# Optimization experiments

Measured on AMD Instinct MI355X. Metric: run time of the kernel, lower is better.

## Reference

```python
import jax, jax.numpy as jnp
import numpy as np

NH = 16  # attention heads
TOPK = 50

def _rms(x, w):
    return x * jax.lax.rsqrt(jnp.mean(x * x, axis=-1, keepdims=True) + 1e-6) * w

def _rope(x, pos):
    # x: [1, T, NH, HD], pos: [T]
    half = x.shape[-1] // 2
    inv = 1.0 / (10000.0 ** (jnp.arange(half, dtype=jnp.float32) / half))
    ang = pos.astype(jnp.float32)[:, None] * inv[None, :]          # [T, half]
    cos = jnp.cos(ang)[None, :, None, :]
    sin = jnp.sin(ang)[None, :, None, :]
    x1, x2 = x[..., :half], x[..., half:]
    return jnp.concatenate([x1 * cos - x2 * sin, x2 * cos + x1 * sin], axis=-1)


def setup_inputs() -> dict:
    key = jax.random.key(0)
    ks = jax.random.split(key, 12)
    G, V, D, NL, FF = 15, 2048, 1024, 2, 4096
    s = 0.02
    return {
        'talker_hidden': jax.random.normal(ks[0], (1, 1, D), jnp.float32),
        'code_0_embed': jax.random.normal(ks[1], (1, 1, D), jnp.float32),
        'temperature': jnp.ones((1,), jnp.float32),
        'sample_uniforms': jax.random.uniform(ks[2], (G,), jnp.float32),
        'stacked_heads': jax.random.normal(ks[3], (G, V, D), jnp.float32) * s,
        'stacked_embeds': jax.random.normal(ks[4], (G, V, D), jnp.float32) * s,
        'ln1': jnp.ones((NL, D), jnp.float32),
        'ln2': jnp.ones((NL, D), jnp.float32),
        'ln_f': jnp.ones((D,), jnp.float32),
        'wq': jax.random.normal(ks[5], (NL, D, D), jnp.float32) * s,
        'wk': jax.random.normal(ks[6], (NL, D, D), jnp.float32) * s,
        'wv': jax.random.normal(ks[7], (NL, D, D), jnp.float32) * s,
        'wo': jax.random.normal(ks[8], (NL, D, D), jnp.float32) * s,
        'w1': jax.random.normal(ks[9], (NL, D, FF), jnp.float32) * s,
        'w2': jax.random.normal(ks[10], (NL, FF, D), jnp.float32) * s,
    }


def reference(talker_hidden, code_0_embed, temperature, sample_uniforms,
              stacked_heads, stacked_embeds, ln1, ln2, ln_f,
              wq, wk, wv, wo, w1, w2):
    NL = wq.shape[0]
    D = wq.shape[1]
    HD = D // NH
    G = stacked_heads.shape[0]

    def transformer_step(h, qpos, caches):
        # h: [1, T, D]; qpos: [T] absolute positions; caches: list of (k,v) or None
        new_caches = []
        for l in range(NL):
            T = h.shape[1]
            x = _rms(h, ln1[l])
            q = (x @ wq[l]).reshape(1, T, NH, HD)
            k = (x @ wk[l]).reshape(1, T, NH, HD)
            v = (x @ wv[l]).reshape(1, T, NH, HD)
            q = _rope(q, qpos)
            k = _rope(k, qpos)
            if caches is None:
                k_all, v_all = k, v
            else:
                k_all = jnp.concatenate([caches[l][0], k], axis=1)
                v_all = jnp.concatenate([caches[l][1], v], axis=1)
            new_caches.append((k_all, v_all))
            S = k_all.shape[1]
            scores = jnp.einsum('bthd,bshd->bhts', q, k_all) / jnp.sqrt(jnp.float32(HD))
            mask = jnp.arange(S)[None, :] <= qpos[:, None]      # [T, S] causal
            scores = jnp.where(mask[None, None], scores, jnp.float32(-1e30))
            attn = jax.nn.softmax(scores, axis=-1)
            out = jnp.einsum('bhts,bshd->bthd', attn, v_all).reshape(1, T, D)
            h = h + out @ wo[l]
            h = h + jax.nn.gelu((_rms(h, ln2[l])) @ w1[l]) @ w2[l]
        return _rms(h, ln_f), new_caches

    cp_input = jnp.concatenate([talker_hidden, code_0_embed], axis=1)  # [1, 2, D]
    h_seq, caches = transformer_step(cp_input, jnp.arange(2), None)
    hidden = h_seq[:, -1:, :]                                           # [1, 1, D]

    safe_temp = jnp.maximum(temperature.reshape(()), 1e-5)
    embed_sum = code_0_embed.reshape(-1)
    codes = []
    for g in range(G):
        logits = stacked_heads[g] @ hidden.reshape(-1)                  # [V]
        topv, topi = jax.lax.top_k(logits, TOPK)
        probs = jax.nn.softmax(topv / safe_temp)
        cdf = jnp.cumsum(probs)
        u = jnp.clip(sample_uniforms[g], 1e-6, 1.0 - 1e-6)
        choice = jnp.argmax((cdf >= u).astype(jnp.int32))
        code = topi[choice]
        codes.append(code.astype(jnp.int64))
        emb = stacked_embeds[g][code]                                   # [D]
        embed_sum = embed_sum + emb
        if g + 1 < G:
            h_seq, caches = transformer_step(emb[None, None, :],
                                             jnp.array([g + 2]), caches)
            hidden = h_seq[:, -1:, :]
    return jnp.stack(codes), embed_sum
```

## Files before the change

### kernel.cpp

```cpp
#include <hip/hip_runtime.h>
#include <math.h>

#define D      1024
#define NHEADS 16
#define HDIM   64
#define NL     2
#define FF     4096
#define NGRP   15
#define VOC    2048
#define TOPK   50
#define MAXS   16

__device__ __forceinline__ float wave_reduce_sum(float v) {
#pragma unroll
    for (int m = 32; m >= 1; m >>= 1) v += __shfl_xor(v, m, 64);
    return v;
}

__device__ __forceinline__ float geluf(float y) {
    return 0.5f * y * (1.f + tanhf(0.7978845608028654f * (y + 0.044715f * y * y * y)));
}

__device__ __forceinline__ void load_rms(const float* __restrict__ src,
                                         const float* __restrict__ w,
                                         float* xn, float* red) {
    int tid = threadIdx.x;
    float ss = 0.f;
    for (int i = tid; i < D; i += 256) { float v = src[i]; xn[i] = v; ss += v * v; }
    red[tid] = ss;
    __syncthreads();
    for (int s = 128; s > 0; s >>= 1) {
        if (tid < s) red[tid] += red[tid + s];
        __syncthreads();
    }
    float inv = rsqrtf(red[0] / (float)D + 1e-6f);
    for (int i = tid; i < D; i += 256) xn[i] = xn[i] * inv * w[i];
    __syncthreads();
}

__global__ void k_init(const float* __restrict__ th, const float* __restrict__ c0,
                       float* __restrict__ h, float* __restrict__ out,
                       float* __restrict__ qkv) {
    int i = blockIdx.x * 256 + threadIdx.x;
    h[i] = th[i];
    h[D + i] = c0[i];
    out[NGRP + i] = c0[i];
#pragma unroll
    for (int j = 0; j < 6; ++j) qkv[j * 1024 + i] = 0.f;
}

__global__ void k_qkv(const float* __restrict__ h, const float* __restrict__ ln,
                      const float* __restrict__ Wq, const float* __restrict__ Wk,
                      const float* __restrict__ Wv, float* __restrict__ qkv) {
    __shared__ float xn[D];
    __shared__ float red[256];
    __shared__ float4 part[4][64];
    int t = blockIdx.z;
    int m = blockIdx.x >> 2, ob = blockIdx.x & 3;
    load_rms(h + t * D, ln, xn, red);
    const float* W = (m == 0) ? Wq : (m == 1) ? Wk : Wv;
    int tid = threadIdx.x, w = tid >> 6, lane = tid & 63;
    int obase = ob * 256;
    int kbase = (blockIdx.y * 4 + w) * 32;
    const float* Wp = W + (long)kbase * D + obase + lane * 4;
    float4 acc = {0.f, 0.f, 0.f, 0.f};
#pragma unroll 4
    for (int i = 0; i < 32; ++i) {
        float xv = xn[kbase + i];
        float4 wv = *(const float4*)(Wp + (long)i * D);
        acc.x += xv * wv.x; acc.y += xv * wv.y; acc.z += xv * wv.z; acc.w += xv * wv.w;
    }
    part[w][lane] = acc;
    __syncthreads();
    const float* p = (const float*)part;
    float s = p[tid] + p[256 + tid] + p[512 + tid] + p[768 + tid];
    atomicAdd(&qkv[t * 3 * D + m * D + obase + tid], s);
}

__global__ void k_attn(const float* __restrict__ qkv, float* __restrict__ kc,
                       float* __restrict__ vc, float* __restrict__ ao,
                       float* __restrict__ ub, int basePos) {
    int t = blockIdx.x, hd = blockIdx.y, d = threadIdx.x;
    {
        int fb = blockIdx.x * NHEADS + blockIdx.y;
#pragma unroll
        for (int j = 0; j < 4; ++j) ub[fb * 256 + j * 64 + d] = 0.f;
    }
    int pos = basePos + t;
    int i = d & 31;
    float inv = __expf(-(float)i * (9.210340371976184f / 32.0f));
    float ang = (float)pos * inv;
    float cs = cosf(ang), sn = sinf(ang);

    float q = qkv[t * 3 * D + hd * HDIM + d];
    float qp = __shfl_xor(q, 32, 64);
    float qr = (d < 32) ? (q * cs - qp * sn) : (q * cs + qp * sn);

    float k0 = qkv[t * 3 * D + D + hd * HDIM + d];
    float kp = __shfl_xor(k0, 32, 64);
    float kr = (d < 32) ? (k0 * cs - kp * sn) : (k0 * cs + kp * sn);

    float v0 = qkv[t * 3 * D + 2 * D + hd * HDIM + d];
    kc[pos * D + hd * HDIM + d] = kr;
    vc[pos * D + hd * HDIM + d] = v0;

    float sc[MAXS];
#pragma unroll
    for (int s = 0; s < MAXS; ++s) {
        if (s > pos) break;
        float kv;
        if (s < basePos) {
            kv = kc[s * D + hd * HDIM + d];
        } else if (s == pos) {
            kv = kr;
        } else {
            float kk = qkv[(s - basePos) * 3 * D + D + hd * HDIM + d];
            float kkp = __shfl_xor(kk, 32, 64);
            float a2 = (float)s * inv;
            float c2 = cosf(a2), s2 = sinf(a2);
            kv = (d < 32) ? (kk * c2 - kkp * s2) : (kk * c2 + kkp * s2);
        }
        float dt = wave_reduce_sum(qr * kv);
        sc[s] = dt * 0.125f;
    }
    float mx = -1e30f;
#pragma unroll
    for (int s = 0; s < MAXS; ++s) { if (s > pos) break; mx = fmaxf(mx, sc[s]); }
    float l = 0.f;
#pragma unroll
    for (int s = 0; s < MAXS; ++s) { if (s > pos) break; sc[s] = expf(sc[s] - mx); l += sc[s]; }
    float o = 0.f;
#pragma unroll
    for (int s = 0; s < MAXS; ++s) {
        if (s > pos) break;
        float vv = (s < basePos) ? vc[s * D + hd * HDIM + d]
                                 : qkv[(s - basePos) * 3 * D + 2 * D + hd * HDIM + d];
        o += sc[s] * vv;
    }
    ao[t * D + hd * HDIM + d] = o / l;
}

__global__ void k_wo(const float* __restrict__ ain, const float* __restrict__ W,
                     float* __restrict__ h, float* __restrict__ qkv) {
    __shared__ float xn[D];
    __shared__ float4 part[4][64];
    int t = blockIdx.z, tid = threadIdx.x;
    if (blockIdx.x == 0 && tid < 192)
        qkv[t * 3 * D + blockIdx.y * 192 + tid] = 0.f;
    for (int i = tid; i < D; i += 256) xn[i] = ain[t * D + i];
    __syncthreads();
    int w = tid >> 6, lane = tid & 63;
    int obase = blockIdx.x * 256;
    int kbase = (blockIdx.y * 4 + w) * 16;
    const float* Wp = W + (long)kbase * D + obase + lane * 4;
    float4 acc = {0.f, 0.f, 0.f, 0.f};
#pragma unroll 4
    for (int i = 0; i < 16; ++i) {
        float xv = xn[kbase + i];
        float4 wv = *(const float4*)(Wp + (long)i * D);
        acc.x += xv * wv.x; acc.y += xv * wv.y; acc.z += xv * wv.z; acc.w += xv * wv.w;
    }
    part[w][lane] = acc;
    __syncthreads();
    const float* p = (const float*)part;
    float s = p[tid] + p[256 + tid] + p[512 + tid] + p[768 + tid];
    atomicAdd(&h[t * D + obase + tid], s);
}

__global__ void k_ffn1(const float* __restrict__ h, const float* __restrict__ ln,
                       const float* __restrict__ W, float* __restrict__ ub) {
    __shared__ float xn[D];
    __shared__ float red[256];
    __shared__ float4 part[4][64];
    int t = blockIdx.z, tid = threadIdx.x;
    load_rms(h + t * D, ln, xn, red);
    int w = tid >> 6, lane = tid & 63;
    int obase = blockIdx.x * 256;
    int kbase = (blockIdx.y * 4 + w) * 32;
    const float* Wp = W + (long)kbase * FF + obase + lane * 4;
    float4 acc = {0.f, 0.f, 0.f, 0.f};
#pragma unroll 4
    for (int i = 0; i < 32; ++i) {
        float xv = xn[kbase + i];
        float4 wv = *(const float4*)(Wp + (long)i * FF);
        acc.x += xv * wv.x; acc.y += xv * wv.y; acc.z += xv * wv.z; acc.w += xv * wv.w;
    }
    part[w][lane] = acc;
    __syncthreads();
    const float* p = (const float*)part;
    float s = p[tid] + p[256 + tid] + p[512 + tid] + p[768 + tid];
    atomicAdd(&ub[t * FF + obase + tid], s);
}

__global__ void k_ffn2(const float* __restrict__ ub, const float* __restrict__ W,
                       float* __restrict__ h) {
    __shared__ float xs[128];
    __shared__ float4 part[4][64];
    int t = blockIdx.z, tid = threadIdx.x;
    int kblk = blockIdx.y * 128;
    if (tid < 128) xs[tid] = geluf(ub[t * FF + kblk + tid]);
    __syncthreads();
    int w = tid >> 6, lane = tid & 63;
    int obase = blockIdx.x * 256;
    int kloc = w * 32;
    const float* Wp = W + (long)(kblk + kloc) * D + obase + lane * 4;
    float4 acc = {0.f, 0.f, 0.f, 0.f};
#pragma unroll 4
    for (int i = 0; i < 32; ++i) {
        float xv = xs[kloc + i];
        float4 wv = *(const float4*)(Wp + (long)i * D);
        acc.x += xv * wv.x; acc.y += xv * wv.y; acc.z += xv * wv.z; acc.w += xv * wv.w;
    }
    part[w][lane] = acc;
    __syncthreads();
    const float* p = (const float*)part;
    float s = p[tid] + p[256 + tid] + p[512 + tid] + p[768 + tid];
    atomicAdd(&h[t * D + obase + tid], s);
}

__global__ void k_head(const float* __restrict__ h, const float* __restrict__ lnf,
                       const float* __restrict__ Hd, float* __restrict__ logits) {
    __shared__ float xn[D];
    __shared__ float red[256];
    load_rms(h, lnf, xn, red);
    int tid = threadIdx.x, lane = tid & 63, w = tid >> 6;
    int rbase = blockIdx.x * 16 + w * 4;
#pragma unroll
    for (int r = 0; r < 4; ++r) {
        const float* row = Hd + (long)(rbase + r) * D;
        float acc = 0.f;
#pragma unroll
        for (int it = 0; it < 4; ++it) {
            int idx = it * 256 + lane * 4;
            float4 a = *(const float4*)(row + idx);
            acc += a.x * xn[idx] + a.y * xn[idx + 1] + a.z * xn[idx + 2] + a.w * xn[idx + 3];
        }
        acc = wave_reduce_sum(acc);
        if (lane == 0) logits[rbase + r] = acc;
    }
}

__global__ void k_sample(const float* __restrict__ logits, const float* __restrict__ temp,
                         const float* __restrict__ unis, const float* __restrict__ embeds,
                         int g, float* __restrict__ h, float* __restrict__ out) {
    __shared__ float topv[TOPK];
    __shared__ int topi[TOPK];
    __shared__ int s_code;
    int tid = threadIdx.x;
    if (tid < 64) {
        int lane = tid;
        float v[32];
#pragma unroll
        for (int j = 0; j < 32; ++j) v[j] = logits[j * 64 + lane];
        for (int r = 0; r < TOPK; ++r) {
            float bv = v[0];
            int bj = 0;
#pragma unroll
            for (int j = 1; j < 32; ++j)
                if (v[j] > bv) { bv = v[j]; bj = j; }
            int bidx = bj * 64 + lane;
#pragma unroll
            for (int m = 32; m >= 1; m >>= 1) {
                float ov = __shfl_xor(bv, m, 64);
                int oi = __shfl_xor(bidx, m, 64);
                if (ov > bv || (ov == bv && oi < bidx)) { bv = ov; bidx = oi; }
            }
            if (lane == 0) { topv[r] = bv; topi[r] = bidx; }
            if ((bidx & 63) == lane) v[bidx >> 6] = -3.0e38f;
        }
    }
    __syncthreads();
    if (tid == 0) {
        float t = fmaxf(temp[0], 1e-5f);
        float m = topv[0] / t;
        float p[TOPK];
        float l = 0.f;
        for (int j = 0; j < TOPK; ++j) { p[j] = expf(topv[j] / t - m); l += p[j]; }
        float u = unis[g];
        u = fminf(fmaxf(u, 1e-6f), 1.f - 1e-6f);
        float cdf = 0.f;
        int choice = 0;
        bool found = false;
        for (int j = 0; j < TOPK; ++j) {
            cdf += p[j] / l;
            if (!found && cdf >= u) { choice = j; found = true; }
        }
        s_code = topi[choice];
        out[g] = (float)s_code;
    }
    __syncthreads();
    int code = s_code;
    const float* e = embeds + ((long)g * VOC + code) * D;
    for (int i = tid; i < D; i += 256) {
        float ev = e[i];
        out[NGRP + i] += ev;
        h[i] = ev;
    }
}

extern "C" void kernel_launch(void* const* d_in, const int* in_sizes, int n_in,
                              void* d_out, int out_size, void* d_ws, size_t ws_size,
                              hipStream_t stream) {
    const float* talker = (const float*)d_in[0];
    const float* code0  = (const float*)d_in[1];
    const float* temp   = (const float*)d_in[2];
    const float* unis   = (const float*)d_in[3];
    const float* heads  = (const float*)d_in[4];
    const float* embeds = (const float*)d_in[5];
    const float* ln1    = (const float*)d_in[6];
    const float* ln2    = (const float*)d_in[7];
    const float* lnf    = (const float*)d_in[8];
    const float* wq     = (const float*)d_in[9];
    const float* wk     = (const float*)d_in[10];
    const float* wv     = (const float*)d_in[11];
    const float* wo     = (const float*)d_in[12];
    const float* w1     = (const float*)d_in[13];
    const float* w2     = (const float*)d_in[14];
    float* out = (float*)d_out;

    float* ws   = (float*)d_ws;
    float* h    = ws;
    float* qkvb = ws + 2048;
    float* ao   = ws + 8192;
    float* kc   = ws + 10240;
    float* vc   = ws + 43008;
    float* ub   = ws + 75776;
    float* lg   = ws + 83968;

    auto step = [&](int T, int basePos) {
        for (int l = 0; l < NL; ++l) {
            k_qkv<<<dim3(12, 8, T), 256, 0, stream>>>(h, ln1 + l * D,
                wq + (long)l * D * D, wk + (long)l * D * D, wv + (long)l * D * D, qkvb);
            k_attn<<<dim3(T, NHEADS), 64, 0, stream>>>(qkvb, kc + (long)l * MAXS * D,
                vc + (long)l * MAXS * D, ao, ub, basePos);
            k_wo<<<dim3(4, 16, T), 256, 0, stream>>>(ao, wo + (long)l * D * D, h, qkvb);
            k_ffn1<<<dim3(16, 8, T), 256, 0, stream>>>(h, ln2 + l * D, w1 + (long)l * D * FF, ub);
            k_ffn2<<<dim3(4, 32, T), 256, 0, stream>>>(ub, w2 + (long)l * FF * D, h);
        }
    };

    k_init<<<4, 256, 0, stream>>>(talker, code0, h, out, qkvb);
    step(2, 0);
    for (int g = 0; g < NGRP; ++g) {
        const float* hid = h + ((g == 0) ? 1 : 0) * D;
        k_head<<<128, 256, 0, stream>>>(hid, lnf, heads + (long)g * VOC * D, lg);
        k_sample<<<1, 256, 0, stream>>>(lg, temp, unis, embeds, g, h, out);
        if (g + 1 < NGRP) step(1, g + 2);
    }
}
```

Measured before the change: 2.392 ms.

## Fuse all decoder steps into one persistent kernel with grid barriers

Replaces roughly 190 small kernel launches (five per layer per step plus head and sample per group) with a single persistent 256-block kernel. Stages are separated by an atomic-counter grid barrier instead of kernel boundaries. The aim is to remove launch overhead and inter-kernel gaps in this latency-bound decode loop. The trade-offs are that 256 co-resident blocks are required for the spin barrier not to deadlock, each barrier costs global atomics and spinning, and the sampling stage leaves most blocks idle.

```diff
diff --git a/kernel.cpp b/kernel.cpp
--- a/kernel.cpp
+++ b/kernel.cpp
@@ -10,6 +10,16 @@
 #define VOC    2048
 #define TOPK   50
 #define MAXS   16
+#define NB     256
+
+struct Params {
+    const float* talker; const float* code0; const float* temp; const float* unis;
+    const float* heads;  const float* embeds;
+    const float* ln1; const float* ln2; const float* lnf;
+    const float* wq; const float* wk; const float* wv; const float* wo;
+    const float* w1; const float* w2;
+    float* out; float* ws;
+};
 
 __device__ __forceinline__ float wave_reduce_sum(float v) {
 #pragma unroll
@@ -19,6 +29,18 @@
 
 __device__ __forceinline__ float geluf(float y) {
     return 0.5f * y * (1.f + tanhf(0.7978845608028654f * (y + 0.044715f * y * y * y)));
+}
+
+__device__ __forceinline__ void gsync(unsigned* cnt, unsigned target) {
+    __syncthreads();
+    if (threadIdx.x == 0) {
+        __threadfence();
+        atomicAdd(cnt, 1u);
+        while (__hip_atomic_load(cnt, __ATOMIC_RELAXED, __HIP_MEMORY_SCOPE_AGENT) < target)
+            __builtin_amdgcn_s_sleep(1);
+        __threadfence();
+    }
+    __syncthreads();
 }
 
 __device__ __forceinline__ void load_rms(const float* __restrict__ src,
@@ -38,263 +60,296 @@
     __syncthreads();
 }
 
-__global__ void k_init(const float* __restrict__ th, const float* __restrict__ c0,
-                       float* __restrict__ h, float* __restrict__ out,
-                       float* __restrict__ qkv) {
+__global__ __launch_bounds__(256) void k_pre(const float* __restrict__ th,
+                                             const float* __restrict__ c0,
+                                             float* __restrict__ h,
+                                             float* __restrict__ out,
+                                             float* __restrict__ qkv,
+                                             unsigned* __restrict__ bar) {
     int i = blockIdx.x * 256 + threadIdx.x;
-    h[i] = th[i];
-    h[D + i] = c0[i];
-    out[NGRP + i] = c0[i];
-#pragma unroll
-    for (int j = 0; j < 6; ++j) qkv[j * 1024 + i] = 0.f;
-}
-
-__global__ void k_qkv(const float* __restrict__ h, const float* __restrict__ ln,
-                      const float* __restrict__ Wq, const float* __restrict__ Wk,
-                      const float* __restrict__ Wv, float* __restrict__ qkv) {
+    if (i == 0) *bar = 0u;
+    if (i < 1024) {
+        h[i] = th[i];
+        h[D + i] = c0[i];
+        out[NGRP + i] = c0[i];
+    }
+    for (int j = i; j < 2 * 3 * D; j += 2048) qkv[j] = 0.f;
+}
+
+__global__ __launch_bounds__(256) void k_all(Params p) {
     __shared__ float xn[D];
     __shared__ float red[256];
     __shared__ float4 part[4][64];
-    int t = blockIdx.z;
-    int m = blockIdx.x >> 2, ob = blockIdx.x & 3;
-    load_rms(h + t * D, ln, xn, red);
-    const float* W = (m == 0) ? Wq : (m == 1) ? Wk : Wv;
-    int tid = threadIdx.x, w = tid >> 6, lane = tid & 63;
-    int obase = ob * 256;
-    int kbase = (blockIdx.y * 4 + w) * 32;
-    const float* Wp = W + (long)kbase * D + obase + lane * 4;
-    float4 acc = {0.f, 0.f, 0.f, 0.f};
+    __shared__ float s_topv[TOPK];
+    __shared__ int   s_topi[TOPK];
+    __shared__ int   s_code;
+
+    float* ws   = p.ws;
+    float* h    = ws;
+    float* qkvb = ws + 2048;
+    float* ao   = ws + 8192;
+    float* kc   = ws + 10240;
+    float* vc   = ws + 43008;
+    float* ub   = ws + 75776;
+    float* lg   = ws + 83968;
+    unsigned* bar = (unsigned*)(ws + 86016);
+
+    const int bid = blockIdx.x;
+    const int tid = threadIdx.x;
+    unsigned bt = 0;
+
+    auto step = [&](int T, int basePos) {
+        for (int l = 0; l < NL; ++l) {
+            if (bid < 96 * T) {
+                int x = bid % 12, y = (bid / 12) % 8, t = bid / 96;
+                int m = x >> 2, ob = x & 3;
+                load_rms(h + t * D, p.ln1 + l * D, xn, red);
+                const float* W = ((m == 0) ? p.wq : (m == 1) ? p.wk : p.wv) + (long)l * D * D;
+                int w = tid >> 6, lane = tid & 63;
+                int obase = ob * 256;
+                int kbase = (y * 4 + w) * 32;
+                const float* Wp = W + (long)kbase * D + obase + lane * 4;
+                float4 acc = {0.f, 0.f, 0.f, 0.f};
 #pragma unroll 4
-    for (int i = 0; i < 32; ++i) {
-        float xv = xn[kbase + i];
-        float4 wv = *(const float4*)(Wp + (long)i * D);
-        acc.x += xv * wv.x; acc.y += xv * wv.y; acc.z += xv * wv.z; acc.w += xv * wv.w;
-    }
-    part[w][lane] = acc;
-    __syncthreads();
-    const float* p = (const float*)part;
-    float s = p[tid] + p[256 + tid] + p[512 + tid] + p[768 + tid];
-    atomicAdd(&qkv[t * 3 * D + m * D + obase + tid], s);
-}
-
-__global__ void k_attn(const float* __restrict__ qkv, float* __restrict__ kc,
-                       float* __restrict__ vc, float* __restrict__ ao,
-                       float* __restrict__ ub, int basePos) {
-    int t = blockIdx.x, hd = blockIdx.y, d = threadIdx.x;
-    {
-        int fb = blockIdx.x * NHEADS + blockIdx.y;
-#pragma unroll
-        for (int j = 0; j < 4; ++j) ub[fb * 256 + j * 64 + d] = 0.f;
-    }
-    int pos = basePos + t;
-    int i = d & 31;
-    float inv = __expf(-(float)i * (9.210340371976184f / 32.0f));
-    float ang = (float)pos * inv;
-    float cs = cosf(ang), sn = sinf(ang);
-
-    float q = qkv[t * 3 * D + hd * HDIM + d];
-    float qp = __shfl_xor(q, 32, 64);
-    float qr = (d < 32) ? (q * cs - qp * sn) : (q * cs + qp * sn);
-
-    float k0 = qkv[t * 3 * D + D + hd * HDIM + d];
-    float kp = __shfl_xor(k0, 32, 64);
-    float kr = (d < 32) ? (k0 * cs - kp * sn) : (k0 * cs + kp * sn);
-
-    float v0 = qkv[t * 3 * D + 2 * D + hd * HDIM + d];
-    kc[pos * D + hd * HDIM + d] = kr;
-    vc[pos * D + hd * HDIM + d] = v0;
-
-    float sc[MAXS];
-#pragma unroll
-    for (int s = 0; s < MAXS; ++s) {
-        if (s > pos) break;
-        float kv;
-        if (s < basePos) {
-            kv = kc[s * D + hd * HDIM + d];
-        } else if (s == pos) {
-            kv = kr;
-        } else {
-            float kk = qkv[(s - basePos) * 3 * D + D + hd * HDIM + d];
-            float kkp = __shfl_xor(kk, 32, 64);
-            float a2 = (float)s * inv;
-            float c2 = cosf(a2), s2 = sinf(a2);
-            kv = (d < 32) ? (kk * c2 - kkp * s2) : (kk * c2 + kkp * s2);
+                for (int i = 0; i < 32; ++i) {
+                    float xv = xn[kbase + i];
+                    float4 wv4 = *(const float4*)(Wp + (long)i * D);
+                    acc.x += xv * wv4.x; acc.y += xv * wv4.y;
+                    acc.z += xv * wv4.z; acc.w += xv * wv4.w;
+                }
+                part[w][lane] = acc;
+                __syncthreads();
+                const float* pp = (const float*)part;
+                float s = pp[tid] + pp[256 + tid] + pp[512 + tid] + pp[768 + tid];
+                atomicAdd(&qkvb[t * 3 * D + m * D + obase + tid], s);
+            }
+            gsync(bar, bt += NB);
+
+            {
+                for (int i = bid * 256 + tid; i < T * FF; i += NB * 256) ub[i] = 0.f;
+                int wid = bid * 4 + (tid >> 6);
+                if (wid < T * NHEADS) {
+                    int t = wid / NHEADS, hd = wid % NHEADS, d = tid & 63;
+                    float* kcl = kc + (long)l * MAXS * D;
+                    float* vcl = vc + (long)l * MAXS * D;
+                    int pos = basePos + t;
+                    int i = d & 31;
+                    float inv = __expf(-(float)i * (9.210340371976184f / 32.0f));
+                    float ang = (float)pos * inv;
+                    float cs = cosf(ang), sn = sinf(ang);
+
+                    float q = qkvb[t * 3 * D + hd * HDIM + d];
+                    float qp = __shfl_xor(q, 32, 64);
+                    float qr = (d < 32) ? (q * cs - qp * sn) : (q * cs + qp * sn);
+
+                    float k0 = qkvb[t * 3 * D + D + hd * HDIM + d];
+                    float kp = __shfl_xor(k0, 32, 64);
+                    float kr = (d < 32) ? (k0 * cs - kp * sn) : (k0 * cs + kp * sn);
+
+                    float v0 = qkvb[t * 3 * D + 2 * D + hd * HDIM + d];
+                    kcl[pos * D + hd * HDIM + d] = kr;
+                    vcl[pos * D + hd * HDIM + d] = v0;
+
+                    float sc[MAXS];
+#pragma unroll
+                    for (int s = 0; s < MAXS; ++s) {
+                        if (s > pos) break;
+                        float kv;
+                        if (s < basePos) {
+                            kv = kcl[s * D + hd * HDIM + d];
+                        } else if (s == pos) {
+                            kv = kr;
+                        } else {
+                            float kk = qkvb[(s - basePos) * 3 * D + D + hd * HDIM + d];
+                            float kkp = __shfl_xor(kk, 32, 64);
+                            float a2 = (float)s * inv;
+                            float c2 = cosf(a2), s2 = sinf(a2);
+                            kv = (d < 32) ? (kk * c2 - kkp * s2) : (kk * c2 + kkp * s2);
+                        }
+                        float dt = wave_reduce_sum(qr * kv);
+                        sc[s] = dt * 0.125f;
+                    }
+                    float mx = -1e30f;
+#pragma unroll
+                    for (int s = 0; s < MAXS; ++s) { if (s > pos) break; mx = fmaxf(mx, sc[s]); }
+                    float lsum = 0.f;
+#pragma unroll
+                    for (int s = 0; s < MAXS; ++s) { if (s > pos) break; sc[s] = expf(sc[s] - mx); lsum += sc[s]; }
+                    float o = 0.f;
+#pragma unroll
+                    for (int s = 0; s < MAXS; ++s) {
+                        if (s > pos) break;
+                        float vv = (s < basePos) ? vcl[s * D + hd * HDIM + d]
+                                                 : qkvb[(s - basePos) * 3 * D + 2 * D + hd * HDIM + d];
+                        o += sc[s] * vv;
+                    }
+                    ao[t * D + hd * HDIM + d] = o / lsum;
+                }
+            }
+            gsync(bar, bt += NB);
+
+            {
+                for (int i = bid * 256 + tid; i < T * 3 * D; i += NB * 256) qkvb[i] = 0.f;
+                if (bid < 64 * T) {
+                    int x = bid % 4, y = (bid / 4) % 16, t = bid / 64;
+                    const float* W = p.wo + (long)l * D * D;
+                    for (int i = tid; i < D; i += 256) xn[i] = ao[t * D + i];
+                    __syncthreads();
+                    int w = tid >> 6, lane = tid & 63;
+                    int obase = x * 256;
+                    int kbase = (y * 4 + w) * 16;
+                    const float* Wp = W + (long)kbase * D + obase + lane * 4;
+                    float4 acc = {0.f, 0.f, 0.f, 0.f};
+#pragma unroll 4
+                    for (int i = 0; i < 16; ++i) {
+                        float xv = xn[kbase + i];
+                        float4 wv4 = *(const float4*)(Wp + (long)i * D);
+                        acc.x += xv * wv4.x; acc.y += xv * wv4.y;
+                        acc.z += xv * wv4.z; acc.w += xv * wv4.w;
+                    }
+                    part[w][lane] = acc;
+                    __syncthreads();
+                    const float* pp = (const float*)part;
+                    float s = pp[tid] + pp[256 + tid] + pp[512 + tid] + pp[768 + tid];
+                    atomicAdd(&h[t * D + obase + tid], s);
+                }
+            }
+            gsync(bar, bt += NB);
+
+            if (bid < 128 * T) {
+                int x = bid % 16, y = (bid / 16) % 8, t = bid / 128;
+                load_rms(h + t * D, p.ln2 + l * D, xn, red);
+                const float* W = p.w1 + (long)l * D * FF;
+                int w = tid >> 6, lane = tid & 63;
+                int obase = x * 256;
+                int kbase = (y * 4 + w) * 32;
+                const float* Wp = W + (long)kbase * FF + obase + lane * 4;
+                float4 acc = {0.f, 0.f, 0.f, 0.f};
+#pragma unroll 4
+                for (int i = 0; i < 32; ++i) {
+                    float xv = xn[kbase + i];
+                    float4 wv4 = *(const float4*)(Wp + (long)i * FF);
+                    acc.x += xv * wv4.x; acc.y += xv * wv4.y;
+                    acc.z += xv * wv4.z; acc.w += xv * wv4.w;
+                }
+                part[w][lane] = acc;
+                __syncthreads();
+                const float* pp = (const float*)part;
+                float s = pp[tid] + pp[256 + tid] + pp[512 + tid] + pp[768 + tid];
+                atomicAdd(&ub[t * FF + obase + tid], s);
+            }
+            gsync(bar, bt += NB);
+
+            if (bid < 128 * T) {
+                int x = bid % 4, y = (bid / 4) % 32, t = bid / 128;
+                int kblk = y * 128;
+                if (tid < 128) red[tid] = geluf(ub[t * FF + kblk + tid]);
+                __syncthreads();
+                const float* W = p.w2 + (long)l * FF * D;
+                int w = tid >> 6, lane = tid & 63;
+                int obase = x * 256;
+                int kloc = w * 32;
+                const float* Wp = W + (long)(kblk + kloc) * D + obase + lane * 4;
+                float4 acc = {0.f, 0.f, 0.f, 0.f};
+#pragma unroll 4
+                for (int i = 0; i < 32; ++i) {
+                    float xv = red[kloc + i];
+                    float4 wv4 = *(const float4*)(Wp + (long)i * D);
+                    acc.x += xv * wv4.x; acc.y += xv * wv4.y;
+                    acc.z += xv * wv4.z; acc.w += xv * wv4.w;
+                }
+                part[w][lane] = acc;
+                __syncthreads();
+                const float* pp = (const float*)part;
+                float s = pp[tid] + pp[256 + tid] + pp[512 + tid] + pp[768 + tid];
+                atomicAdd(&h[t * D + obase + tid], s);
+            }
+            gsync(bar, bt += NB);
         }
-        float dt = wave_reduce_sum(qr * kv);
-        sc[s] = dt * 0.125f;
-    }
-    float mx = -1e30f;
-#pragma unroll
-    for (int s = 0; s < MAXS; ++s) { if (s > pos) break; mx = fmaxf(mx, sc[s]); }
-    float l = 0.f;
-#pragma unroll
-    for (int s = 0; s < MAXS; ++s) { if (s > pos) break; sc[s] = expf(sc[s] - mx); l += sc[s]; }
-    float o = 0.f;
-#pragma unroll
-    for (int s = 0; s < MAXS; ++s) {
-        if (s > pos) break;
-        float vv = (s < basePos) ? vc[s * D + hd * HDIM + d]
-                                 : qkv[(s - basePos) * 3 * D + 2 * D + hd * HDIM + d];
-        o += sc[s] * vv;
-    }
-    ao[t * D + hd * HDIM + d] = o / l;
-}
-
-__global__ void k_wo(const float* __restrict__ ain, const float* __restrict__ W,
-                     float* __restrict__ h, float* __restrict__ qkv) {
-    __shared__ float xn[D];
-    __shared__ float4 part[4][64];
-    int t = blockIdx.z, tid = threadIdx.x;
-    if (blockIdx.x == 0 && tid < 192)
-        qkv[t * 3 * D + blockIdx.y * 192 + tid] = 0.f;
-    for (int i = tid; i < D; i += 256) xn[i] = ain[t * D + i];
-    __syncthreads();
-    int w = tid >> 6, lane = tid & 63;
-    int obase = blockIdx.x * 256;
-    int kbase = (blockIdx.y * 4 + w) * 16;
-    const float* Wp = W + (long)kbase * D + obase + lane * 4;
-    float4 acc = {0.f, 0.f, 0.f, 0.f};
-#pragma unroll 4
-    for (int i = 0; i < 16; ++i) {
-        float xv = xn[kbase + i];
-        float4 wv = *(const float4*)(Wp + (long)i * D);
-        acc.x += xv * wv.x; acc.y += xv * wv.y; acc.z += xv * wv.z; acc.w += xv * wv.w;
-    }
-    part[w][lane] = acc;
-    __syncthreads();
-    const float* p = (const float*)part;
-    float s = p[tid] + p[256 + tid] + p[512 + tid] + p[768 + tid];
-    atomicAdd(&h[t * D + obase + tid], s);
-}
-
-__global__ void k_ffn1(const float* __restrict__ h, const float* __restrict__ ln,
-                       const float* __restrict__ W, float* __restrict__ ub) {
-    __shared__ float xn[D];
-    __shared__ float red[256];
-    __shared__ float4 part[4][64];
-    int t = blockIdx.z, tid = threadIdx.x;
-    load_rms(h + t * D, ln, xn, red);
-    int w = tid >> 6, lane = tid & 63;
-    int obase = blockIdx.x * 256;
-    int kbase = (blockIdx.y * 4 + w) * 32;
-    const float* Wp = W + (long)kbase * FF + obase + lane * 4;
-    float4 acc = {0.f, 0.f, 0.f, 0.f};
-#pragma unroll 4
-    for (int i = 0; i < 32; ++i) {
-        float xv = xn[kbase + i];
-        float4 wv = *(const float4*)(Wp + (long)i * FF);
-        acc.x += xv * wv.x; acc.y += xv * wv.y; acc.z += xv * wv.z; acc.w += xv * wv.w;
-    }
-    part[w][lane] = acc;
-    __syncthreads();
-    const float* p = (const float*)part;
-    float s = p[tid] + p[256 + tid] + p[512 + tid] + p[768 + tid];
-    atomicAdd(&ub[t * FF + obase + tid], s);
-}
-
-__global__ void k_ffn2(const float* __restrict__ ub, const float* __restrict__ W,
-                       float* __restrict__ h) {
-    __shared__ float xs[128];
-    __shared__ float4 part[4][64];
-    int t = blockIdx.z, tid = threadIdx.x;
-    int kblk = blockIdx.y * 128;
-    if (tid < 128) xs[tid] = geluf(ub[t * FF + kblk + tid]);
-    __syncthreads();
-    int w = tid >> 6, lane = tid & 63;
-    int obase = blockIdx.x * 256;
-    int kloc = w * 32;
-    const float* Wp = W + (long)(kblk + kloc) * D + obase + lane * 4;
-    float4 acc = {0.f, 0.f, 0.f, 0.f};
-#pragma unroll 4
-    for (int i = 0; i < 32; ++i) {
-        float xv = xs[kloc + i];
-        float4 wv = *(const float4*)(Wp + (long)i * D);
-        acc.x += xv * wv.x; acc.y += xv * wv.y; acc.z += xv * wv.z; acc.w += xv * wv.w;
-    }
-    part[w][lane] = acc;
-    __syncthreads();
-    const float* p = (const float*)part;
-    float s = p[tid] + p[256 + tid] + p[512 + tid] + p[768 + tid];
-    atomicAdd(&h[t * D + obase + tid], s);
-}
-
-__global__ void k_head(const float* __restrict__ h, const float* __restrict__ lnf,
-                       const float* __restrict__ Hd, float* __restrict__ logits) {
-    __shared__ float xn[D];
-    __shared__ float red[256];
-    load_rms(h, lnf, xn, red);
-    int tid = threadIdx.x, lane = tid & 63, w = tid >> 6;
-    int rbase = blockIdx.x * 16 + w * 4;
-#pragma unroll
-    for (int r = 0; r < 4; ++r) {
-        const float* row = Hd + (long)(rbase + r) * D;
-        float acc = 0.f;
-#pragma unroll
-        for (int it = 0; it < 4; ++it) {
-            int idx = it * 256 + lane * 4;
-            float4 a = *(const float4*)(row + idx);
-            acc += a.x * xn[idx] + a.y * xn[idx + 1] + a.z * xn[idx + 2] + a.w * xn[idx + 3];
+    };
+
+    step(2, 0);
+
+    for (int g = 0; g < NGRP; ++g) {
+        {
+            const float* hid = h + ((g == 0) ? D : 0);
+            if (bid < 128) {
+                load_rms(hid, p.lnf, xn, red);
+                int lane = tid & 63, w = tid >> 6;
+                int rbase = bid * 16 + w * 4;
+                const float* Hd = p.heads + (long)g * VOC * D;
+#pragma unroll
+                for (int r = 0; r < 4; ++r) {
+                    const float* row = Hd + (long)(rbase + r) * D;
+                    float acc = 0.f;
+#pragma unroll
+                    for (int it = 0; it < 4; ++it) {
+                        int idx = it * 256 + lane * 4;
+                        float4 a = *(const float4*)(row + idx);
+                        acc += a.x * xn[idx] + a.y * xn[idx + 1]
+                             + a.z * xn[idx + 2] + a.w * xn[idx + 3];
+                    }
+                    acc = wave_reduce_sum(acc);
+                    if (lane == 0) lg[rbase + r] = acc;
+                }
+            }
         }
-        acc = wave_reduce_sum(acc);
-        if (lane == 0) logits[rbase + r] = acc;
-    }
-}
-
-__global__ void k_sample(const float* __restrict__ logits, const float* __restrict__ temp,
-                         const float* __restrict__ unis, const float* __restrict__ embeds,
-                         int g, float* __restrict__ h, float* __restrict__ out) {
-    __shared__ float topv[TOPK];
-    __shared__ int topi[TOPK];
-    __shared__ int s_code;
-    int tid = threadIdx.x;
-    if (tid < 64) {
-        int lane = tid;
-        float v[32];
-#pragma unroll
-        for (int j = 0; j < 32; ++j) v[j] = logits[j * 64 + lane];
-        for (int r = 0; r < TOPK; ++r) {
-            float bv = v[0];
-            int bj = 0;
-#pragma unroll
-            for (int j = 1; j < 32; ++j)
-                if (v[j] > bv) { bv = v[j]; bj = j; }
-            int bidx = bj * 64 + lane;
-#pragma unroll
-            for (int m = 32; m >= 1; m >>= 1) {
-                float ov = __shfl_xor(bv, m, 64);
-                int oi = __shfl_xor(bidx, m, 64);
-                if (ov > bv || (ov == bv && oi < bidx)) { bv = ov; bidx = oi; }
-            }
-            if (lane == 0) { topv[r] = bv; topi[r] = bidx; }
-            if ((bidx & 63) == lane) v[bidx >> 6] = -3.0e38f;
+        gsync(bar, bt += NB);
+
+        if (bid == 0) {
+            if (tid < 64) {
+                int lane = tid;
+                float v[32];
+#pragma unroll
+                for (int j = 0; j < 32; ++j) v[j] = lg[j * 64 + lane];
+                for (int r = 0; r < TOPK; ++r) {
+                    float bv = v[0];
+                    int bj = 0;
+#pragma unroll
+                    for (int j = 1; j < 32; ++j)
+                        if (v[j] > bv) { bv = v[j]; bj = j; }
+                    int bidx = bj * 64 + lane;
+#pragma unroll
+                    for (int m = 32; m >= 1; m >>= 1) {
+                        float ov = __shfl_xor(bv, m, 64);
+                        int oi = __shfl_xor(bidx, m, 64);
+                        if (ov > bv || (ov == bv && oi < bidx)) { bv = ov; bidx = oi; }
+                    }
+                    if (lane == 0) { s_topv[r] = bv; s_topi[r] = bidx; }
+                    if ((bidx & 63) == lane) v[bidx >> 6] = -3.0e38f;
+                }
+            }
+            __syncthreads();
+            if (tid == 0) {
+                float t = fmaxf(p.temp[0], 1e-5f);
+                float m = s_topv[0] / t;
+                float pr[TOPK];
+                float l = 0.f;
+                for (int j = 0; j < TOPK; ++j) { pr[j] = expf(s_topv[j] / t - m); l += pr[j]; }
+                float u = p.unis[g];
+                u = fminf(fmaxf(u, 1e-6f), 1.f - 1e-6f);
+                float cdf = 0.f;
+                int choice = 0;
+                bool found = false;
+                for (int j = 0; j < TOPK; ++j) {
+                    cdf += pr[j] / l;
+                    if (!found && cdf >= u) { choice = j; found = true; }
+                }
+                s_code = s_topi[choice];
+                p.out[g] = (float)s_code;
+            }
+            __syncthreads();
+            int code = s_code;
+            const float* e = p.embeds + ((long)g * VOC + code) * D;
+            for (int i = tid; i < D; i += 256) {
+                float ev = e[i];
+                p.out[NGRP + i] += ev;
+                h[i] = ev;
+            }
         }
-    }
-    __syncthreads();
-    if (tid == 0) {
-        float t = fmaxf(temp[0], 1e-5f);
-        float m = topv[0] / t;
-        float p[TOPK];
-        float l = 0.f;
-        for (int j = 0; j < TOPK; ++j) { p[j] = expf(topv[j] / t - m); l += p[j]; }
-        float u = unis[g];
-        u = fminf(fmaxf(u, 1e-6f), 1.f - 1e-6f);
-        float cdf = 0.f;
-        int choice = 0;
-        bool found = false;
-        for (int j = 0; j < TOPK; ++j) {
-            cdf += p[j] / l;
-            if (!found && cdf >= u) { choice = j; found = true; }
-        }
-        s_code = topi[choice];
-        out[g] = (float)s_code;
-    }
-    __syncthreads();
-    int code = s_code;
-    const float* e = embeds + ((long)g * VOC + code) * D;
-    for (int i = tid; i < D; i += 256) {
-        float ev = e[i];
-        out[NGRP + i] += ev;
-        h[i] = ev;
+        gsync(bar, bt += NB);
+
+        if (g + 1 < NGRP) step(1, g + 2);
     }
 }
 
@@ -321,30 +376,11 @@
     float* ws   = (float*)d_ws;
     float* h    = ws;
     float* qkvb = ws + 2048;
-    float* ao   = ws + 8192;
-    float* kc   = ws + 10240;
-    float* vc   = ws + 43008;
-    float* ub   = ws + 75776;
-    float* lg   = ws + 83968;
-
-    auto step = [&](int T, int basePos) {
-        for (int l = 0; l < NL; ++l) {
-            k_qkv<<<dim3(12, 8, T), 256, 0, stream>>>(h, ln1 + l * D,
-                wq + (long)l * D * D, wk + (long)l * D * D, wv + (long)l * D * D, qkvb);
-            k_attn<<<dim3(T, NHEADS), 64, 0, stream>>>(qkvb, kc + (long)l * MAXS * D,
-                vc + (long)l * MAXS * D, ao, ub, basePos);
-            k_wo<<<dim3(4, 16, T), 256, 0, stream>>>(ao, wo + (long)l * D * D, h, qkvb);
-            k_ffn1<<<dim3(16, 8, T), 256, 0, stream>>>(h, ln2 + l * D, w1 + (long)l * D * FF, ub);
-            k_ffn2<<<dim3(4, 32, T), 256, 0, stream>>>(ub, w2 + (long)l * FF * D, h);
-        }
-    };
-
-    k_init<<<4, 256, 0, stream>>>(talker, code0, h, out, qkvb);
-    step(2, 0);
-    for (int g = 0; g < NGRP; ++g) {
-        const float* hid = h + ((g == 0) ? 1 : 0) * D;
-        k_head<<<128, 256, 0, stream>>>(hid, lnf, heads + (long)g * VOC * D, lg);
-        k_sample<<<1, 256, 0, stream>>>(lg, temp, unis, embeds, g, h, out);
-        if (g + 1 < NGRP) step(1, g + 2);
-    }
-}
+    unsigned* bar = (unsigned*)(ws + 86016);
+
+    k_pre<<<8, 256, 0, stream>>>(talker, code0, h, out, qkvb, bar);
+
+    Params pr{talker, code0, temp, unis, heads, embeds, ln1, ln2, lnf,
+              wq, wk, wv, wo, w1, w2, out, ws};
+    k_all<<<dim3(NB), dim3(256), 0, stream>>>(pr);
+}
```

New measurement: 4.613 ms. +92.9%, slower.
